# Kernel tuning notes

Hardware: AMD Instinct MI355X
Metric: run time of the kernel (lower is better)

## Reference

```python
import jax, jax.numpy as jnp
import numpy as np


def setup_inputs() -> dict:
    key = jax.random.key(0)
    k1, k2 = jax.random.split(key)
    B, L, D = 16, 4096, 1024
    X = jax.random.normal(k1, (B, L, D), dtype=jnp.float32)
    G = jax.random.normal(k2, (D, 2), dtype=jnp.float32) * (1.0 / np.sqrt(D))
    Gb = jnp.zeros((2,), dtype=jnp.float32)
    return {"X": X, "G": G, "Gb": Gb}


def reference(X, G, Gb):
    # X: (B, L, D) with L = 2*maxseg. For even i in [0, L-3]:
    #   out_p = X[:,i] * g0 + X[:,i+2] * g1, gates g = softmax(X[:,i+1] @ G + Gb)
    L = X.shape[1]
    lefts = X[:, 0:L - 2:2, :]   # (B, P, D), P = L/2 - 1
    mids = X[:, 1:L - 1:2, :]    # (B, P, D)
    rights = X[:, 2:L:2, :]      # (B, P, D)
    gates = jax.nn.softmax(jnp.einsum('bpd,dg->bpg', mids, G) + Gb, axis=-1)  # (B, P, 2)
    out = lefts * gates[..., 0:1] + rights * gates[..., 1:2]  # (B, P, D)
    return out
```

## Files before the change

kernel.cpp:

```cpp
#include <hip/hip_runtime.h>
#include <hip/hip_bf16.h>

constexpr int B = 16;
constexpr int L = 4096;
constexpr int D = 1024;
constexpr int P = (L - 2) / 2;

constexpr int WAVES_PER_BATCH = 512;
constexpr int CHUNK = 4;

__global__ __launch_bounds__(256) void gated_cnn_kernel(
    const float* __restrict__ X,
    const float* __restrict__ G,
    const float* __restrict__ Gb,
    float* __restrict__ out) {
  const int gtid = blockIdx.x * 256 + threadIdx.x;
  const int wid  = gtid >> 6;
  const int lane = gtid & 63;

  const int b  = wid >> 9;
  const int c  = wid & (WAVES_PER_BATCH - 1);
  const int p0 = c * CHUNK;

  float4 gA[4], gB[4];
  #pragma unroll
  for (int j = 0; j < 4; ++j) {
    const int f4 = j * 64 + lane;
    gA[j] = ((const float4*)G)[2 * f4];
    gB[j] = ((const float4*)G)[2 * f4 + 1];
  }
  const float gb0 = Gb[0];
  const float gb1 = Gb[1];

  const float* xb = X + (size_t)b * L * D;
  float* ob = out + (size_t)b * P * D;

  float4 lf[4];
  {
    const float4* lrow = (const float4*)(xb + (size_t)(2 * p0) * D);
    #pragma unroll
    for (int j = 0; j < 4; ++j) lf[j] = lrow[j * 64 + lane];
  }

  for (int i = 0; i < CHUNK; ++i) {
    const int p = p0 + i;
    if (p >= P) break;

    const float4* mrow = (const float4*)(xb + (size_t)(2 * p + 1) * D);
    const float4* rrow = (const float4*)(xb + (size_t)(2 * p + 2) * D);
    float4 m[4], rt[4];
    #pragma unroll
    for (int j = 0; j < 4; ++j) {
      m[j]  = mrow[j * 64 + lane];
      rt[j] = rrow[j * 64 + lane];
    }

    float s0 = 0.f, s1 = 0.f;
    #pragma unroll
    for (int j = 0; j < 4; ++j) {
      s0 += m[j].x * gA[j].x + m[j].y * gA[j].z + m[j].z * gB[j].x + m[j].w * gB[j].z;
      s1 += m[j].x * gA[j].y + m[j].y * gA[j].w + m[j].z * gB[j].y + m[j].w * gB[j].w;
    }

    #pragma unroll
    for (int off = 1; off < 64; off <<= 1) {
      s0 += __shfl_xor(s0, off, 64);
      s1 += __shfl_xor(s1, off, 64);
    }

    const float t0 = s0 + gb0;
    const float t1 = s1 + gb1;
    const float mx = fmaxf(t0, t1);
    const float e0 = __expf(t0 - mx);
    const float e1 = __expf(t1 - mx);
    const float inv = 1.0f / (e0 + e1);
    const float g0 = e0 * inv;
    const float g1 = e1 * inv;

    float4* orow = (float4*)(ob + (size_t)p * D);
    #pragma unroll
    for (int j = 0; j < 4; ++j) {
      float4 r;
      r.x = lf[j].x * g0 + rt[j].x * g1;
      r.y = lf[j].y * g0 + rt[j].y * g1;
      r.z = lf[j].z * g0 + rt[j].z * g1;
      r.w = lf[j].w * g0 + rt[j].w * g1;
      orow[j * 64 + lane] = r;
      lf[j] = rt[j];
    }
  }
}

extern "C" void kernel_launch(void* const* d_in, const int* in_sizes, int n_in,
                              void* d_out, int out_size, void* d_ws, size_t ws_size,
                              hipStream_t stream) {
  const float* X  = (const float*)d_in[0];
  const float* G  = (const float*)d_in[1];
  const float* Gb = (const float*)d_in[2];
  float* out = (float*)d_out;

  gated_cnn_kernel<<<dim3(B * WAVES_PER_BATCH / 4), dim3(256), 0, stream>>>(X, G, Gb, out);
}
```

Baseline: 388.5 us.

## Split gate computation and blend into separate kernels with batched row loads

Moves the per-pair gate dot product and softmax into a separate kernel that writes gates to workspace. Each gate is reduced over a 16-lane group, so the long 64-lane shuffle chain is gone. The blend kernel then issues all four right-row loads up front, so they are no longer serialized behind a reduction. The cost is an extra launch and reading the mid rows in a separate pass, which adds about a third more X traffic, though those rows may be partly cache-resident.

```diff
diff --git a/kernel.cpp b/kernel.cpp
--- a/kernel.cpp
+++ b/kernel.cpp
@@ -5,89 +5,106 @@
 constexpr int L = 4096;
 constexpr int D = 1024;
 constexpr int P = (L - 2) / 2;
+constexpr int PSLOT = 2048;
 
-constexpr int WAVES_PER_BATCH = 512;
-constexpr int CHUNK = 4;
+__global__ __launch_bounds__(256) void gates_kernel(
+    const float* __restrict__ X, const float* __restrict__ G,
+    const float* __restrict__ Gb, float2* __restrict__ gates) {
+  const int t    = threadIdx.x;
+  const int wave = t >> 6;
+  const int lane = t & 63;
+  const int grp  = lane >> 4;
+  const int l16  = lane & 15;
 
-__global__ __launch_bounds__(256) void gated_cnn_kernel(
-    const float* __restrict__ X,
-    const float* __restrict__ G,
-    const float* __restrict__ Gb,
+  const int b     = blockIdx.x >> 7;
+  const int pbase = (blockIdx.x & 127) * 16;
+  const int p     = pbase + wave * 4 + grp;
+
+  const float4* m4 = (const float4*)(X + ((size_t)b * L + (2 * p + 1)) * D);
+  const float4* g4 = (const float4*)G;
+
+  float4 mbuf[16];
+  #pragma unroll
+  for (int k = 0; k < 16; ++k) mbuf[k] = m4[l16 + 16 * k];
+
+  float s0 = 0.f, s1 = 0.f;
+  #pragma unroll
+  for (int k = 0; k < 16; ++k) {
+    const int f4 = l16 + 16 * k;
+    const float4 ga = g4[2 * f4];
+    const float4 gb = g4[2 * f4 + 1];
+    const float4 m  = mbuf[k];
+    s0 += m.x * ga.x + m.y * ga.z + m.z * gb.x + m.w * gb.z;
+    s1 += m.x * ga.y + m.y * ga.w + m.z * gb.y + m.w * gb.w;
+  }
+
+  #pragma unroll
+  for (int off = 1; off < 16; off <<= 1) {
+    s0 += __shfl_xor(s0, off, 16);
+    s1 += __shfl_xor(s1, off, 16);
+  }
+
+  if (l16 == 0) {
+    const float t0 = s0 + Gb[0];
+    const float t1 = s1 + Gb[1];
+    const float mx = fmaxf(t0, t1);
+    const float e0 = __expf(t0 - mx);
+    const float e1 = __expf(t1 - mx);
+    const float inv = 1.0f / (e0 + e1);
+    gates[b * PSLOT + p] = make_float2(e0 * inv, e1 * inv);
+  }
+}
+
+__global__ __launch_bounds__(256) void blend_kernel(
+    const float* __restrict__ X, const float2* __restrict__ gates,
     float* __restrict__ out) {
   const int gtid = blockIdx.x * 256 + threadIdx.x;
   const int wid  = gtid >> 6;
   const int lane = gtid & 63;
-
-  const int b  = wid >> 9;
-  const int c  = wid & (WAVES_PER_BATCH - 1);
-  const int p0 = c * CHUNK;
-
-  float4 gA[4], gB[4];
-  #pragma unroll
-  for (int j = 0; j < 4; ++j) {
-    const int f4 = j * 64 + lane;
-    gA[j] = ((const float4*)G)[2 * f4];
-    gB[j] = ((const float4*)G)[2 * f4 + 1];
-  }
-  const float gb0 = Gb[0];
-  const float gb1 = Gb[1];
+  const int b    = wid >> 9;
+  const int c    = wid & 511;
+  const int p0   = c * 4;
 
   const float* xb = X + (size_t)b * L * D;
-  float* ob = out + (size_t)b * P * D;
 
   float4 lf[4];
   {
     const float4* lrow = (const float4*)(xb + (size_t)(2 * p0) * D);
     #pragma unroll
-    for (int j = 0; j < 4; ++j) lf[j] = lrow[j * 64 + lane];
+    for (int j = 0; j < 4; ++j) lf[j] = lrow[64 * j + lane];
   }
 
-  for (int i = 0; i < CHUNK; ++i) {
+  float4 rt[4][4];
+  #pragma unroll
+  for (int i = 0; i < 4; ++i) {
+    const int row = min(2 * p0 + 2 * i + 2, L - 1);
+    const float4* rrow = (const float4*)(xb + (size_t)row * D);
+    #pragma unroll
+    for (int j = 0; j < 4; ++j) rt[i][j] = rrow[64 * j + lane];
+  }
+
+  float2 g[4];
+  #pragma unroll
+  for (int i = 0; i < 4; ++i) g[i] = gates[b * PSLOT + p0 + i];
+
+  float* ob = out + (size_t)b * P * D;
+  #pragma unroll
+  for (int i = 0; i < 4; ++i) {
     const int p = p0 + i;
-    if (p >= P) break;
-
-    const float4* mrow = (const float4*)(xb + (size_t)(2 * p + 1) * D);
-    const float4* rrow = (const float4*)(xb + (size_t)(2 * p + 2) * D);
-    float4 m[4], rt[4];
+    if (p < P) {
+      float4* orow = (float4*)(ob + (size_t)p * D);
+      #pragma unroll
+      for (int j = 0; j < 4; ++j) {
+        float4 r;
+        r.x = lf[j].x * g[i].x + rt[i][j].x * g[i].y;
+        r.y = lf[j].y * g[i].x + rt[i][j].y * g[i].y;
+        r.z = lf[j].z * g[i].x + rt[i][j].z * g[i].y;
+        r.w = lf[j].w * g[i].x + rt[i][j].w * g[i].y;
+        orow[64 * j + lane] = r;
+      }
+    }
     #pragma unroll
-    for (int j = 0; j < 4; ++j) {
-      m[j]  = mrow[j * 64 + lane];
-      rt[j] = rrow[j * 64 + lane];
-    }
-
-    float s0 = 0.f, s1 = 0.f;
-    #pragma unroll
-    for (int j = 0; j < 4; ++j) {
-      s0 += m[j].x * gA[j].x + m[j].y * gA[j].z + m[j].z * gB[j].x + m[j].w * gB[j].z;
-      s1 += m[j].x * gA[j].y + m[j].y * gA[j].w + m[j].z * gB[j].y + m[j].w * gB[j].w;
-    }
-
-    #pragma unroll
-    for (int off = 1; off < 64; off <<= 1) {
-      s0 += __shfl_xor(s0, off, 64);
-      s1 += __shfl_xor(s1, off, 64);
-    }
-
-    const float t0 = s0 + gb0;
-    const float t1 = s1 + gb1;
-    const float mx = fmaxf(t0, t1);
-    const float e0 = __expf(t0 - mx);
-    const float e1 = __expf(t1 - mx);
-    const float inv = 1.0f / (e0 + e1);
-    const float g0 = e0 * inv;
-    const float g1 = e1 * inv;
-
-    float4* orow = (float4*)(ob + (size_t)p * D);
-    #pragma unroll
-    for (int j = 0; j < 4; ++j) {
-      float4 r;
-      r.x = lf[j].x * g0 + rt[j].x * g1;
-      r.y = lf[j].y * g0 + rt[j].y * g1;
-      r.z = lf[j].z * g0 + rt[j].z * g1;
-      r.w = lf[j].w * g0 + rt[j].w * g1;
-      orow[j * 64 + lane] = r;
-      lf[j] = rt[j];
-    }
+    for (int j = 0; j < 4; ++j) lf[j] = rt[i][j];
   }
 }
 
@@ -98,6 +115,8 @@
   const float* G  = (const float*)d_in[1];
   const float* Gb = (const float*)d_in[2];
   float* out = (float*)d_out;
+  float2* gates = (float2*)d_ws;
 
-  gated_cnn_kernel<<<dim3(B * WAVES_PER_BATCH / 4), dim3(256), 0, stream>>>(X, G, Gb, out);
+  gates_kernel<<<dim3(B * 128), dim3(256), 0, stream>>>(X, G, Gb, gates);
+  blend_kernel<<<dim3(B * 512 / 4), dim3(256), 0, stream>>>(X, gates, out);
 }
```

Result: no change. 393.0 us (+1.2%).
